# Kernel optimization log

Measured on AMD Instinct MI355X. Metric: run time of the kernel, lower is better.

The kernel has to match this reference:

```python
import jax, jax.numpy as jnp
import numpy as np

B, MAXN, D, H, S = 64, 512, 512, 8, 32
DH = D // H          # per-head dim = 64
N = B * MAXN         # 32768 total nodes
E = 524288           # ~avg degree 16
EPS = 1e-5


def setup_inputs() -> dict:
    key = jax.random.key(0)
    ks = jax.random.split(key, 18)
    s = 0.05
    x_dense = jax.random.normal(ks[0], (B, MAXN, D), jnp.float32)
    x = jax.random.normal(ks[1], (N, D), jnp.float32)
    src = jax.random.randint(ks[2], (E,), 0, N)
    # destinations kept within the same graph as the source
    dst = (src // MAXN) * MAXN + jax.random.randint(ks[3], (E,), 0, MAXN)
    edge_index = jnp.stack([src, dst]).astype(jnp.int32)
    batch = (jnp.arange(N) // MAXN).astype(jnp.int32)  # sorted, 512 nodes/graph
    seed = jax.random.normal(ks[4], (S, 1, D), jnp.float32) * s
    # per-head GCN conv weights concatenated along output dim: [D, H*DH] == [D, D]
    Wk = jax.random.normal(ks[5], (D, D), jnp.float32) * s
    bk = jnp.zeros((D,), jnp.float32)
    Wv = jax.random.normal(ks[6], (D, D), jnp.float32) * s
    bv = jnp.zeros((D,), jnp.float32)
    q_proj_weight = jax.random.normal(ks[7], (D, D), jnp.float32) * s
    Wo = jax.random.normal(ks[8], (D, D), jnp.float32) * s
    bo = jnp.zeros((D,), jnp.float32)
    Wff = jax.random.normal(ks[9], (D, D), jnp.float32) * s
    bff = jnp.zeros((D,), jnp.float32)
    gamma_h = jnp.ones((D,), jnp.float32)
    beta_h = jnp.zeros((D,), jnp.float32)
    gamma_z = jnp.ones((D,), jnp.float32)
    beta_z = jnp.zeros((D,), jnp.float32)
    return dict(x_dense=x_dense, x=x, edge_index=edge_index, batch=batch,
                seed=seed, Wk=Wk, bk=bk, Wv=Wv, bv=bv,
                q_proj_weight=q_proj_weight, Wo=Wo, bo=bo, Wff=Wff, bff=bff,
                gamma_h=gamma_h, beta_h=beta_h, gamma_z=gamma_z, beta_z=beta_z)


def _gcn(x, W, b, src, dst):
    # PyG GCNConv with self-loops + symmetric norm; all H heads fused via W [D, H*DH]
    xw = x @ W                                   # [N, D]
    idx = jnp.arange(N)
    src_f = jnp.concatenate([src, idx])
    dst_f = jnp.concatenate([dst, idx])
    deg = jax.ops.segment_sum(jnp.ones_like(dst_f, dtype=x.dtype), dst_f, num_segments=N)
    dinv = jax.lax.rsqrt(deg)                    # deg >= 1 (self-loops)
    norm = dinv[src_f] * dinv[dst_f]             # [E+N]
    out = jax.ops.segment_sum(xw[src_f] * norm[:, None], dst_f, num_segments=N)
    return out + b


def _to_dense(feat, batch):
    # to_dense_batch for sorted batch vector; padded slots are zeros
    counts = jax.ops.segment_sum(jnp.ones((N,), jnp.int32), batch, num_segments=B)
    start = jnp.cumsum(counts) - counts
    pos = jnp.arange(N) - start[batch]
    return jnp.zeros((B, MAXN, feat.shape[-1]), feat.dtype).at[batch, pos].set(feat)


def _layernorm(x, g, b):
    m = jnp.mean(x, -1, keepdims=True)
    v = jnp.mean(jnp.square(x - m), -1, keepdims=True)
    return (x - m) * jax.lax.rsqrt(v + EPS) * g + b


def reference(x_dense, x, edge_index, batch, seed, Wk, bk, Wv, bv,
              q_proj_weight, Wo, bo, Wff, bff, gamma_h, beta_h, gamma_z, beta_z):
    src, dst = edge_index[0], edge_index[1]
    k_nodes = _gcn(x, Wk, bk, src, dst)          # [N, D] (H heads concat)
    v_nodes = _gcn(x, Wv, bv, src, dst)
    k_dense = _to_dense(k_nodes, batch)          # [B, MAXN, D]
    v_dense = _to_dense(v_nodes, batch)

    # query: seed [S,1,D] repeated over batch -> [S,B,D]; q projection (F.linear)
    query = jnp.broadcast_to(seed, (S, B, D))
    q = jnp.einsum('sbd,ed->sbe', query, q_proj_weight)
    scale = 1.0 / jnp.sqrt(jnp.float32(DH))
    qh = (q * scale).reshape(S, B, H, DH).transpose(1, 2, 0, 3)     # [B,H,S,DH]
    kh = k_dense.reshape(B, MAXN, H, DH).transpose(0, 2, 1, 3)      # [B,H,N,DH]
    vh = v_dense.reshape(B, MAXN, H, DH).transpose(0, 2, 1, 3)
    scores = jnp.einsum('bhsd,bhnd->bhsn', qh, kh)                  # [B,H,S,MAXN]
    attn = jax.nn.softmax(scores, axis=-1)                          # no padding mask (faithful)
    ctx = jnp.einsum('bhsn,bhnd->bhsd', attn, vh)                   # [B,H,S,DH]
    ctx = ctx.transpose(0, 2, 1, 3).reshape(B, S, D)                # heads concat
    attn_out = ctx @ Wo.T + bo                                      # [B,S,D]

    query_bse = jnp.broadcast_to(seed.transpose(1, 0, 2), (B, S, D))
    embed = _layernorm(query_bse + attn_out, gamma_h, beta_h)
    embed = _layernorm(embed + embed @ Wff.T + bff, gamma_z, beta_z)
    return embed
```

## Files before the change

kernel.cpp:

```cpp
#include <hip/hip_runtime.h>
#include <hip/hip_bf16.h>

#define BN   64
#define MAXN 512
#define DIM  512
#define NH   8
#define NS   32
#define NN   32768
#define NE   524288
#define MP   (2048 * 512)

typedef __hip_bfloat16 bf16;
using bf16x8 = __attribute__((ext_vector_type(8))) short;
using f32x4  = __attribute__((ext_vector_type(4))) float;

__device__ int   g_cnt[NN];
__device__ int   g_cur[NN];
__device__ int   g_off[NN + 1];
__device__ int   g_csr[NE];
__device__ float g_dinv[NN];
__device__ bf16  g_xb[NN * DIM];
__device__ bf16  g_agg[NN * DIM];
__device__ bf16  g_aggT[NN * DIM];
__device__ bf16  g_qf[256 * DIM];
__device__ bf16  g_wob[DIM * DIM];
__device__ bf16  g_wvb[DIM * DIM];
__device__ bf16  g_wvo[DIM * 8 * DIM];
__device__ float g_bvo[DIM];
__device__ bf16  g_wffT[DIM * DIM];
__device__ float g_q[NS * DIM];
__device__ bf16  g_sc[BN * 256 * MAXN];
__device__ bf16  g_cp[BN * NS * 8 * DIM];
__device__ float g_part[8 * MP];
__device__ float g_h1[BN * NS * DIM];
__device__ bf16  g_h1b[BN * NS * DIM];

__device__ inline float bf2f(unsigned short u) {
    union { unsigned int i; float f; } x; x.i = ((unsigned int)u) << 16; return x.f;
}

__device__ inline void gll16(const bf16* g, bf16* l) {
    __builtin_amdgcn_global_load_lds(
        (const __attribute__((address_space(1))) void*)g,
        (__attribute__((address_space(3))) void*)l, 16, 0, 0);
}

__global__ void k_zero() {
    int i = blockIdx.x * 256 + threadIdx.x;
    if (i < NN) { g_cnt[i] = 0; g_cur[i] = 0; }
}

__global__ void k_count(const int* __restrict__ dst) {
    int e = blockIdx.x * 256 + threadIdx.x;
    if (e < NE) atomicAdd(&g_cnt[dst[e]], 1);
}

__global__ void k_scan() {
    __shared__ int part[1024];
    int t = threadIdx.x;
    int base = t * 32;
    int loc[32]; int s = 0;
#pragma unroll
    for (int i = 0; i < 32; i++) { loc[i] = g_cnt[base + i]; s += loc[i]; }
    part[t] = s; __syncthreads();
    for (int o = 1; o < 1024; o <<= 1) {
        int v = (t >= o) ? part[t - o] : 0;
        __syncthreads();
        part[t] += v;
        __syncthreads();
    }
    int ex = (t == 0) ? 0 : part[t - 1];
#pragma unroll
    for (int i = 0; i < 32; i++) {
        g_off[base + i] = ex; ex += loc[i];
        g_dinv[base + i] = rsqrtf(1.0f + (float)loc[i]);
    }
    if (t == 1023) g_off[NN] = ex;
}

__global__ void k_fill(const int* __restrict__ src, const int* __restrict__ dst) {
    int e = blockIdx.x * 256 + threadIdx.x;
    if (e < NE) {
        int d = dst[e];
        int p = atomicAdd(&g_cur[d], 1);
        g_csr[g_off[d] + p] = src[e];
    }
}

__global__ __launch_bounds__(256) void k_xb(const float* __restrict__ x) {
    long i = (long)(blockIdx.x * 256 + threadIdx.x) * 8;
    int node = (int)(i >> 9);
    float w = g_dinv[node];
    float4 a = *(const float4*)(x + i);
    float4 b = *(const float4*)(x + i + 4);
    float v[8] = {a.x, a.y, a.z, a.w, b.x, b.y, b.z, b.w};
    bf16x8 o;
#pragma unroll
    for (int j = 0; j < 8; j++) { bf16 t = __float2bfloat16(v[j] * w); o[j] = *(short*)&t; }
    *(bf16x8*)(g_xb + i) = o;
}

__global__ __launch_bounds__(256) void k_gather() {
    int bid = blockIdx.x;
    int lb = (bid & 7) * 1024 + (bid >> 3);
    int wave = threadIdx.x >> 6, lane = threadIdx.x & 63;
    int node = lb * 4 + wave;

    bf16x8 sv = ((const bf16x8*)(g_xb + (long)node * DIM))[lane];
    float acc[8];
#pragma unroll
    for (int j = 0; j < 8; j++) acc[j] = bf2f((unsigned short)sv[j]);

    int e = g_off[node], e1 = g_off[node + 1];
    for (; e + 4 <= e1; e += 4) {
        int s0 = g_csr[e], s1 = g_csr[e + 1], s2 = g_csr[e + 2], s3 = g_csr[e + 3];
        bf16x8 r0 = ((const bf16x8*)(g_xb + (long)s0 * DIM))[lane];
        bf16x8 r1 = ((const bf16x8*)(g_xb + (long)s1 * DIM))[lane];
        bf16x8 r2 = ((const bf16x8*)(g_xb + (long)s2 * DIM))[lane];
        bf16x8 r3 = ((const bf16x8*)(g_xb + (long)s3 * DIM))[lane];
#pragma unroll
        for (int j = 0; j < 8; j++)
            acc[j] += (bf2f((unsigned short)r0[j]) + bf2f((unsigned short)r1[j]))
                    + (bf2f((unsigned short)r2[j]) + bf2f((unsigned short)r3[j]));
    }
    for (; e < e1; e++) {
        int s0 = g_csr[e];
        bf16x8 r0 = ((const bf16x8*)(g_xb + (long)s0 * DIM))[lane];
#pragma unroll
        for (int j = 0; j < 8; j++) acc[j] += bf2f((unsigned short)r0[j]);
    }
    float dd = g_dinv[node];
    bf16x8 o;
#pragma unroll
    for (int j = 0; j < 8; j++) { bf16 t = __float2bfloat16(acc[j] * dd); o[j] = *(short*)&t; }
    ((bf16x8*)(g_agg + (long)node * DIM))[lane] = o;
}

__global__ __launch_bounds__(256) void k_aggT() {
    __shared__ unsigned short L[64][72];
    int id = blockIdx.x;
    int b = id >> 6, t = id & 63;
    int n0 = (t & 7) * 64, d0 = (t >> 3) * 64;
    int tid = threadIdx.x;
    const unsigned short* src = (const unsigned short*)g_agg + ((long)b * 512 + n0) * 512 + d0;
#pragma unroll
    for (int p = 0; p < 2; p++) {
        int r = (tid >> 3) + 32 * p, c = (tid & 7) * 8;
        *(int4*)&L[r][c] = *(const int4*)(src + (long)r * 512 + c);
    }
    __syncthreads();
    unsigned short* dst = (unsigned short*)g_aggT + ((long)b * 512 + d0) * 512 + n0;
#pragma unroll
    for (int p = 0; p < 2; p++) {
        int dr = (tid >> 3) + 32 * p, c0 = (tid & 7) * 8;
        unsigned short tmp[8];
#pragma unroll
        for (int j = 0; j < 8; j++) tmp[j] = L[c0 + j][dr];
        *(int4*)(dst + (long)dr * 512 + c0) = *(int4*)tmp;
    }
}

__global__ void k_qproj(const float* __restrict__ seed, const float* __restrict__ Wq) {
    int i = blockIdx.x * 256 + threadIdx.x;
    int s = i >> 9, e = i & 511;
    const float* sr = seed + s * DIM;
    const float* wr = Wq + e * DIM;
    float a0 = 0.f, a1 = 0.f;
    for (int d = 0; d < DIM; d += 8) {
        float4 a = *(const float4*)(sr + d);
        float4 b = *(const float4*)(wr + d);
        float4 c = *(const float4*)(sr + d + 4);
        float4 w = *(const float4*)(wr + d + 4);
        a0 += a.x * b.x + a.y * b.y + a.z * b.z + a.w * b.w;
        a1 += c.x * w.x + c.y * w.y + c.z * w.z + c.w * w.w;
    }
    g_q[i] = (a0 + a1) * 0.125f;
}

__global__ __launch_bounds__(256) void k_cvt(const float* __restrict__ Wo,
                                             const float* __restrict__ Wv,
                                             const float* __restrict__ Wff) {
    long t = blockIdx.x * 256 + threadIdx.x;
    const float* src; bf16* dst; long off;
    if (t < 32768)      { src = Wo;  dst = g_wob;  off = t; }
    else if (t < 65536) { src = Wv;  dst = g_wvb;  off = t - 32768; }
    else                { src = Wff; dst = g_wffT; off = t - 65536; }
    long i = off * 8;
    float4 a = *(const float4*)(src + i);
    float4 b = *(const float4*)(src + i + 4);
    float v[8] = {a.x, a.y, a.z, a.w, b.x, b.y, b.z, b.w};
    bf16x8 o;
#pragma unroll
    for (int j = 0; j < 8; j++) { bf16 q = __float2bfloat16(v[j]); o[j] = *(short*)&q; }
    *(bf16x8*)(dst + i) = o;
}

__global__ __launch_bounds__(256) void k_qf(const float* __restrict__ Wk) {
    int i = blockIdx.x * 256 + threadIdx.x;
    int hs = i >> 9, d = i & 511;
    int h = hs >> 5, s = hs & 31;
    const float* qr = g_q + s * DIM + h * 64;
    const float* wr = Wk + d * DIM + h * 64;
    float a0 = 0.f, a1 = 0.f;
    for (int t2 = 0; t2 < 64; t2 += 8) {
        float4 a = *(const float4*)(qr + t2);
        float4 w = *(const float4*)(wr + t2);
        float4 c = *(const float4*)(qr + t2 + 4);
        float4 u = *(const float4*)(wr + t2 + 4);
        a0 += a.x * w.x + a.y * w.y + a.z * w.z + a.w * w.w;
        a1 += c.x * u.x + c.y * u.y + c.z * u.z + c.w * u.w;
    }
    g_qf[i] = __float2bfloat16(a0 + a1);
}

__global__ __launch_bounds__(256) void k_bvo(const float* __restrict__ bo,
                                             const float* __restrict__ bv,
                                             const float* __restrict__ Wo) {
    int e = blockIdx.x * 256 + threadIdx.x;
    const float* orow = Wo + (long)e * DIM;
    float a0 = 0.f, a1 = 0.f;
    for (int c = 0; c < DIM; c += 8) {
        float4 a = *(const float4*)(bv + c);
        float4 w = *(const float4*)(orow + c);
        float4 x = *(const float4*)(bv + c + 4);
        float4 u = *(const float4*)(orow + c + 4);
        a0 += a.x * w.x + a.y * w.y + a.z * w.z + a.w * w.w;
        a1 += x.x * u.x + x.y * u.y + x.z * u.z + x.w * u.w;
    }
    g_bvo[e] = bo[e] + a0 + a1;
}

__device__ __forceinline__ void gemm128(const bf16* __restrict__ A, long lda,
                                        const bf16* __restrict__ Bt, long ldb,
                                        long row0, long col0, int kbeg, int kend,
                                        bf16 (*As)[128 * 32], bf16 (*Bs)[128 * 32],
                                        f32x4 acc[4][4]) {
    int tid = threadIdx.x;
    int lane = tid & 63, wave = tid >> 6;
    int wr = wave >> 1, wc = wave & 1;
    int fr = lane & 15, fq = lane >> 4;
    int rchunk = (fq ^ ((fr >> 1) & 3)) * 8;
    int u0 = wave * 128 + lane;
    int sr0 = u0 >> 2, sc0 = ((u0 & 3) ^ ((sr0 >> 1) & 3)) * 8;
    int u1 = u0 + 64;
    int sr1 = u1 >> 2, sc1 = ((u1 & 3) ^ ((sr1 >> 1) & 3)) * 8;

    auto stage = [&](int buf, int kt) {
        gll16(A + (row0 + sr0) * lda + kt + sc0, As[buf] + u0 * 8);
        gll16(A + (row0 + sr1) * lda + kt + sc1, As[buf] + u1 * 8);
        gll16(Bt + (col0 + sr0) * ldb + kt + sc0, Bs[buf] + u0 * 8);
        gll16(Bt + (col0 + sr1) * ldb + kt + sc1, Bs[buf] + u1 * 8);
    };

    stage(0, kbeg);
    __syncthreads();
    for (int kt = kbeg; kt < kend; kt += 32) {
        int buf = ((kt - kbeg) >> 5) & 1;
        if (kt + 32 < kend) stage(buf ^ 1, kt + 32);
        bf16x8 af[4], bfv[4];
#pragma unroll
        for (int mi = 0; mi < 4; mi++)
            af[mi] = *(const bf16x8*)(As[buf] + (wr * 64 + mi * 16 + fr) * 32 + rchunk);
#pragma unroll
        for (int ni = 0; ni < 4; ni++)
            bfv[ni] = *(const bf16x8*)(Bs[buf] + (wc * 64 + ni * 16 + fr) * 32 + rchunk);
#pragma unroll
        for (int mi = 0; mi < 4; mi++)
#pragma unroll
            for (int ni = 0; ni < 4; ni++)
                acc[mi][ni] = __builtin_amdgcn_mfma_f32_16x16x32_bf16(af[mi], bfv[ni], acc[mi][ni], 0, 0, 0);
        __syncthreads();
    }
}

#define GEMM_PROLOGUE                                        \
    __shared__ bf16 As[2][128 * 32];                         \
    __shared__ bf16 Bs[2][128 * 32];                         \
    f32x4 acc[4][4];                                         \
    _Pragma("unroll")                                        \
    for (int i = 0; i < 4; i++)                              \
        _Pragma("unroll")                                    \
        for (int j = 0; j < 4; j++) acc[i][j] = (f32x4){0.f, 0.f, 0.f, 0.f}; \
    int lane = threadIdx.x & 63, wave = threadIdx.x >> 6;    \
    int wr = wave >> 1, wc = wave & 1;                       \
    int fr = lane & 15, fq = lane >> 4;

__global__ __launch_bounds__(256) void k_wvo() {
    GEMM_PROLOGUE
    int h = blockIdx.z;
    long row0 = (long)blockIdx.x * 128, col0 = (long)blockIdx.y * 128;
    gemm128(g_wob, DIM, g_wvb, DIM, row0, col0, h * 64, h * 64 + 64, As, Bs, acc);
#pragma unroll
    for (int mi = 0; mi < 4; mi++)
#pragma unroll
        for (int ni = 0; ni < 4; ni++) {
            long col = col0 + wc * 64 + ni * 16 + fr;
#pragma unroll
            for (int r = 0; r < 4; r++) {
                long row = row0 + wr * 64 + mi * 16 + fq * 4 + r;
                g_wvo[row * 4096 + h * 512 + col] = __float2bfloat16(acc[mi][ni][r]);
            }
        }
}

__global__ __launch_bounds__(256) void k_scores() {
    GEMM_PROLOGUE
    int b = blockIdx.z;
    long row0 = (long)blockIdx.x * 128, col0 = (long)blockIdx.y * 128;
    gemm128(g_qf, DIM, g_agg + (long)b * (MAXN * DIM), DIM, row0, col0, 0, DIM, As, Bs, acc);
    bf16* out = g_sc + (long)b * (256 * MAXN);
#pragma unroll
    for (int mi = 0; mi < 4; mi++)
#pragma unroll
        for (int ni = 0; ni < 4; ni++) {
            long col = col0 + wc * 64 + ni * 16 + fr;
#pragma unroll
            for (int r = 0; r < 4; r++) {
                long row = row0 + wr * 64 + mi * 16 + fq * 4 + r;
                out[row * MAXN + col] = __float2bfloat16(acc[mi][ni][r]);
            }
        }
}

__global__ __launch_bounds__(256) void k_soft() {
    int w = threadIdx.x >> 6, lane = threadIdx.x & 63;
    unsigned short* base = (unsigned short*)g_sc + ((long)blockIdx.x * 16 + w * 4) * MAXN;
#pragma unroll
    for (int r = 0; r < 4; r++) {
        unsigned short* row = base + (long)r * MAXN;
        float v[8]; float m = -1e30f;
#pragma unroll
        for (int k = 0; k < 8; k++) { v[k] = bf2f(row[lane + 64 * k]); m = fmaxf(m, v[k]); }
#pragma unroll
        for (int o = 32; o > 0; o >>= 1) m = fmaxf(m, __shfl_xor(m, o));
        float sum = 0.f;
#pragma unroll
        for (int k = 0; k < 8; k++) { v[k] = __expf(v[k] - m); sum += v[k]; }
#pragma unroll
        for (int o = 32; o > 0; o >>= 1) sum += __shfl_xor(sum, o);
        float inv = 1.0f / sum;
#pragma unroll
        for (int k = 0; k < 8; k++) {
            bf16 t = __float2bfloat16(v[k] * inv);
            row[lane + 64 * k] = *(unsigned short*)&t;
        }
    }
}

__global__ __launch_bounds__(256) void k_pvg() {
    GEMM_PROLOGUE
    int z = blockIdx.z, b = z >> 1, dh = z & 1;
    long row0 = (long)blockIdx.x * 128, col0 = (long)blockIdx.y * 128;
    gemm128(g_sc + (long)b * (256 * MAXN), MAXN,
            g_aggT + (long)b * (DIM * MAXN) + (long)dh * (256 * MAXN), MAXN,
            row0, col0, 0, MAXN, As, Bs, acc);
#pragma unroll
    for (int mi = 0; mi < 4; mi++)
#pragma unroll
        for (int ni = 0; ni < 4; ni++) {
            long col = col0 + wc * 64 + ni * 16 + fr;
#pragma unroll
            for (int r = 0; r < 4; r++) {
                long row = row0 + wr * 64 + mi * 16 + fq * 4 + r;
                g_cp[((long)b * NS + (row & 31)) * 4096 + (row >> 5) * 512 + dh * 256 + col] =
                    __float2bfloat16(acc[mi][ni][r]);
            }
        }
}

__global__ __launch_bounds__(256) void k_vo() {
    GEMM_PROLOGUE
    int z = blockIdx.z;
    long row0 = (long)blockIdx.x * 128, col0 = (long)blockIdx.y * 128;
    gemm128(g_cp, 4096, g_wvo, 4096, row0, col0, z * 512, z * 512 + 512, As, Bs, acc);
    float* out = g_part + (long)z * MP;
#pragma unroll
    for (int mi = 0; mi < 4; mi++)
#pragma unroll
        for (int ni = 0; ni < 4; ni++) {
            long col = col0 + wc * 64 + ni * 16 + fr;
#pragma unroll
            for (int r = 0; r < 4; r++) {
                long row = row0 + wr * 64 + mi * 16 + fq * 4 + r;
                out[row * DIM + col] = acc[mi][ni][r];
            }
        }
}

__global__ __launch_bounds__(256) void k_ffn() {
    GEMM_PROLOGUE
    int z = blockIdx.z;
    long row0 = (long)blockIdx.x * 128, col0 = (long)blockIdx.y * 128;
    gemm128(g_h1b, DIM, g_wffT, DIM, row0, col0, z * 128, z * 128 + 128, As, Bs, acc);
    float* out = g_part + (long)z * MP;
#pragma unroll
    for (int mi = 0; mi < 4; mi++)
#pragma unroll
        for (int ni = 0; ni < 4; ni++) {
            long col = col0 + wc * 64 + ni * 16 + fr;
#pragma unroll
            for (int r = 0; r < 4; r++) {
                long row = row0 + wr * 64 + mi * 16 + fq * 4 + r;
                out[row * DIM + col] = acc[mi][ni][r];
            }
        }
}

__device__ inline float blockReduceSum(float v, float* red, int tid) {
#pragma unroll
    for (int o = 32; o > 0; o >>= 1) v += __shfl_xor(v, o);
    __syncthreads();
    if ((tid & 63) == 0) red[tid >> 6] = v;
    __syncthreads();
    return red[0] + red[1] + red[2] + red[3];
}

__global__ __launch_bounds__(256) void k_ln1(const float* __restrict__ seed,
                                             const float* __restrict__ gamma,
                                             const float* __restrict__ beta) {
    __shared__ float red[4];
    int r = blockIdx.x, t = threadIdx.x;
    int s = r & 31;
    long base = (long)r * DIM;
    float v0 = seed[s * DIM + t] + g_bvo[t];
    float v1 = seed[s * DIM + 256 + t] + g_bvo[256 + t];
#pragma unroll
    for (int z = 0; z < 8; z++) {
        v0 += g_part[(long)z * MP + base + t];
        v1 += g_part[(long)z * MP + base + 256 + t];
    }
    float mean = blockReduceSum(v0 + v1, red, t) * (1.0f / DIM);
    float d0 = v0 - mean, d1 = v1 - mean;
    float var = blockReduceSum(d0 * d0 + d1 * d1, red, t) * (1.0f / DIM);
    float ri = rsqrtf(var + 1e-5f);
    float o0 = d0 * ri * gamma[t] + beta[t];
    float o1 = d1 * ri * gamma[256 + t] + beta[256 + t];
    g_h1[base + t] = o0; g_h1[base + 256 + t] = o1;
    g_h1b[base + t] = __float2bfloat16(o0);
    g_h1b[base + 256 + t] = __float2bfloat16(o1);
}

__global__ __launch_bounds__(256) void k_ln2(const float* __restrict__ gamma,
                                             const float* __restrict__ beta,
                                             const float* __restrict__ bff,
                                             float* __restrict__ out) {
    __shared__ float red[4];
    int r = blockIdx.x, t = threadIdx.x;
    long base = (long)r * DIM;
    float v0 = g_h1[base + t] + bff[t];
    float v1 = g_h1[base + 256 + t] + bff[256 + t];
#pragma unroll
    for (int z = 0; z < 4; z++) {
        v0 += g_part[(long)z * MP + base + t];
        v1 += g_part[(long)z * MP + base + 256 + t];
    }
    float mean = blockReduceSum(v0 + v1, red, t) * (1.0f / DIM);
    float d0 = v0 - mean, d1 = v1 - mean;
    float var = blockReduceSum(d0 * d0 + d1 * d1, red, t) * (1.0f / DIM);
    float ri = rsqrtf(var + 1e-5f);
    out[base + t] = d0 * ri * gamma[t] + beta[t];
    out[base + 256 + t] = d1 * ri * gamma[256 + t] + beta[256 + t];
}

extern "C" void kernel_launch(void* const* d_in, const int* in_sizes, int n_in,
                              void* d_out, int out_size, void* d_ws, size_t ws_size,
                              hipStream_t stream) {
    (void)in_sizes; (void)n_in; (void)out_size; (void)d_ws; (void)ws_size;
    const float* x    = (const float*)d_in[1];
    const int*   ei   = (const int*)d_in[2];
    const int*   esrc = ei;
    const int*   edst = ei + NE;
    const float* seed = (const float*)d_in[4];
    const float* Wk   = (const float*)d_in[5];
    const float* Wv   = (const float*)d_in[7];
    const float* bv   = (const float*)d_in[8];
    const float* Wq   = (const float*)d_in[9];
    const float* Wo   = (const float*)d_in[10];
    const float* bo   = (const float*)d_in[11];
    const float* Wff  = (const float*)d_in[12];
    const float* bff  = (const float*)d_in[13];
    const float* gh   = (const float*)d_in[14];
    const float* bh   = (const float*)d_in[15];
    const float* gz   = (const float*)d_in[16];
    const float* bz   = (const float*)d_in[17];
    float* out = (float*)d_out;

    k_zero <<<NN / 256, 256, 0, stream>>>();
    k_count<<<NE / 256, 256, 0, stream>>>(edst);
    k_scan <<<1, 1024, 0, stream>>>();
    k_fill <<<NE / 256, 256, 0, stream>>>(esrc, edst);
    k_xb   <<<(NN * DIM) / (256 * 8), 256, 0, stream>>>(x);
    k_gather<<<NN / 4, 256, 0, stream>>>();
    k_aggT <<<BN * 64, 256, 0, stream>>>();
    k_qproj<<<(NS * DIM) / 256, 256, 0, stream>>>(seed, Wq);
    k_cvt  <<<384, 256, 0, stream>>>(Wo, Wv, Wff);
    k_qf   <<<512, 256, 0, stream>>>(Wk);
    k_wvo  <<<dim3(4, 4, 8), 256, 0, stream>>>();
    k_bvo  <<<2, 256, 0, stream>>>(bo, bv, Wo);

    k_scores<<<dim3(2, 4, BN), 256, 0, stream>>>();
    k_soft  <<<1024, 256, 0, stream>>>();
    k_pvg   <<<dim3(2, 2, BN * 2), 256, 0, stream>>>();

    k_vo <<<dim3(16, 4, 8), 256, 0, stream>>>();
    k_ln1<<<BN * NS, 256, 0, stream>>>(seed, gh, bh);
    k_ffn<<<dim3(16, 4, 4), 256, 0, stream>>>();
    k_ln2<<<BN * NS, 256, 0, stream>>>(gz, bz, bff, out);
}
```

Baseline: 270.5 us.

## Merge independent prep kernels into combined launches and halve split-K partials

Independent small kernels are merged into single launches that branch on block index: edge counting with q-projection, weight conversion and bias folding; CSR fill with x scaling, qf and the Wv·Wo GEMM; scores GEMM with the agg transpose. This cuts launch count and serialization gaps between tiny kernels. The k_vo split-K factor drops from 8 to 4, which halves partial-sum traffic in ln1 but lengthens each block's K loop. The gather loop is unrolled to 8 neighbours to raise memory-level parallelism.

```diff
diff --git a/kernel.cpp b/kernel.cpp
--- a/kernel.cpp
+++ b/kernel.cpp
@@ -31,7 +31,7 @@
 __device__ float g_q[NS * DIM];
 __device__ bf16  g_sc[BN * 256 * MAXN];
 __device__ bf16  g_cp[BN * NS * 8 * DIM];
-__device__ float g_part[8 * MP];
+__device__ float g_part[4 * MP];
 __device__ float g_h1[BN * NS * DIM];
 __device__ bf16  g_h1b[BN * NS * DIM];
 
@@ -50,9 +50,61 @@
     if (i < NN) { g_cnt[i] = 0; g_cur[i] = 0; }
 }
 
-__global__ void k_count(const int* __restrict__ dst) {
-    int e = blockIdx.x * 256 + threadIdx.x;
-    if (e < NE) atomicAdd(&g_cnt[dst[e]], 1);
+__global__ __launch_bounds__(256) void k_cntprep(const int* __restrict__ dst,
+                                                 const float* __restrict__ seed,
+                                                 const float* __restrict__ Wq,
+                                                 const float* __restrict__ Wo,
+                                                 const float* __restrict__ Wv,
+                                                 const float* __restrict__ Wff,
+                                                 const float* __restrict__ bo,
+                                                 const float* __restrict__ bv) {
+    int blk = blockIdx.x;
+    if (blk < 2048) {
+        int e = blk * 256 + threadIdx.x;
+        atomicAdd(&g_cnt[dst[e]], 1);
+    } else if (blk < 2112) {
+        int i = (blk - 2048) * 256 + threadIdx.x;
+        int s = i >> 9, e = i & 511;
+        const float* sr = seed + s * DIM;
+        const float* wr = Wq + e * DIM;
+        float a0 = 0.f, a1 = 0.f;
+        for (int d = 0; d < DIM; d += 8) {
+            float4 a = *(const float4*)(sr + d);
+            float4 b = *(const float4*)(wr + d);
+            float4 c = *(const float4*)(sr + d + 4);
+            float4 w = *(const float4*)(wr + d + 4);
+            a0 += a.x * b.x + a.y * b.y + a.z * b.z + a.w * b.w;
+            a1 += c.x * w.x + c.y * w.y + c.z * w.z + c.w * w.w;
+        }
+        g_q[i] = (a0 + a1) * 0.125f;
+    } else if (blk < 2496) {
+        long t = (long)(blk - 2112) * 256 + threadIdx.x;
+        const float* src; bf16* dstp; long off;
+        if (t < 32768)      { src = Wo;  dstp = g_wob;  off = t; }
+        else if (t < 65536) { src = Wv;  dstp = g_wvb;  off = t - 32768; }
+        else                { src = Wff; dstp = g_wffT; off = t - 65536; }
+        long i = off * 8;
+        float4 a = *(const float4*)(src + i);
+        float4 b = *(const float4*)(src + i + 4);
+        float v[8] = {a.x, a.y, a.z, a.w, b.x, b.y, b.z, b.w};
+        bf16x8 o;
+#pragma unroll
+        for (int j = 0; j < 8; j++) { bf16 q = __float2bfloat16(v[j]); o[j] = *(short*)&q; }
+        *(bf16x8*)(dstp + i) = o;
+    } else {
+        int e = (blk - 2496) * 256 + threadIdx.x;
+        const float* orow = Wo + (long)e * DIM;
+        float a0 = 0.f, a1 = 0.f;
+        for (int c = 0; c < DIM; c += 8) {
+            float4 a = *(const float4*)(bv + c);
+            float4 w = *(const float4*)(orow + c);
+            float4 xx = *(const float4*)(bv + c + 4);
+            float4 u = *(const float4*)(orow + c + 4);
+            a0 += a.x * w.x + a.y * w.y + a.z * w.z + a.w * w.w;
+            a1 += xx.x * u.x + xx.y * u.y + xx.z * u.z + xx.w * u.w;
+        }
+        g_bvo[e] = bo[e] + a0 + a1;
+    }
 }
 
 __global__ void k_scan() {
@@ -76,158 +128,6 @@
         g_dinv[base + i] = rsqrtf(1.0f + (float)loc[i]);
     }
     if (t == 1023) g_off[NN] = ex;
-}
-
-__global__ void k_fill(const int* __restrict__ src, const int* __restrict__ dst) {
-    int e = blockIdx.x * 256 + threadIdx.x;
-    if (e < NE) {
-        int d = dst[e];
-        int p = atomicAdd(&g_cur[d], 1);
-        g_csr[g_off[d] + p] = src[e];
-    }
-}
-
-__global__ __launch_bounds__(256) void k_xb(const float* __restrict__ x) {
-    long i = (long)(blockIdx.x * 256 + threadIdx.x) * 8;
-    int node = (int)(i >> 9);
-    float w = g_dinv[node];
-    float4 a = *(const float4*)(x + i);
-    float4 b = *(const float4*)(x + i + 4);
-    float v[8] = {a.x, a.y, a.z, a.w, b.x, b.y, b.z, b.w};
-    bf16x8 o;
-#pragma unroll
-    for (int j = 0; j < 8; j++) { bf16 t = __float2bfloat16(v[j] * w); o[j] = *(short*)&t; }
-    *(bf16x8*)(g_xb + i) = o;
-}
-
-__global__ __launch_bounds__(256) void k_gather() {
-    int bid = blockIdx.x;
-    int lb = (bid & 7) * 1024 + (bid >> 3);
-    int wave = threadIdx.x >> 6, lane = threadIdx.x & 63;
-    int node = lb * 4 + wave;
-
-    bf16x8 sv = ((const bf16x8*)(g_xb + (long)node * DIM))[lane];
-    float acc[8];
-#pragma unroll
-    for (int j = 0; j < 8; j++) acc[j] = bf2f((unsigned short)sv[j]);
-
-    int e = g_off[node], e1 = g_off[node + 1];
-    for (; e + 4 <= e1; e += 4) {
-        int s0 = g_csr[e], s1 = g_csr[e + 1], s2 = g_csr[e + 2], s3 = g_csr[e + 3];
-        bf16x8 r0 = ((const bf16x8*)(g_xb + (long)s0 * DIM))[lane];
-        bf16x8 r1 = ((const bf16x8*)(g_xb + (long)s1 * DIM))[lane];
-        bf16x8 r2 = ((const bf16x8*)(g_xb + (long)s2 * DIM))[lane];
-        bf16x8 r3 = ((const bf16x8*)(g_xb + (long)s3 * DIM))[lane];
-#pragma unroll
-        for (int j = 0; j < 8; j++)
-            acc[j] += (bf2f((unsigned short)r0[j]) + bf2f((unsigned short)r1[j]))
-                    + (bf2f((unsigned short)r2[j]) + bf2f((unsigned short)r3[j]));
-    }
-    for (; e < e1; e++) {
-        int s0 = g_csr[e];
-        bf16x8 r0 = ((const bf16x8*)(g_xb + (long)s0 * DIM))[lane];
-#pragma unroll
-        for (int j = 0; j < 8; j++) acc[j] += bf2f((unsigned short)r0[j]);
-    }
-    float dd = g_dinv[node];
-    bf16x8 o;
-#pragma unroll
-    for (int j = 0; j < 8; j++) { bf16 t = __float2bfloat16(acc[j] * dd); o[j] = *(short*)&t; }
-    ((bf16x8*)(g_agg + (long)node * DIM))[lane] = o;
-}
-
-__global__ __launch_bounds__(256) void k_aggT() {
-    __shared__ unsigned short L[64][72];
-    int id = blockIdx.x;
-    int b = id >> 6, t = id & 63;
-    int n0 = (t & 7) * 64, d0 = (t >> 3) * 64;
-    int tid = threadIdx.x;
-    const unsigned short* src = (const unsigned short*)g_agg + ((long)b * 512 + n0) * 512 + d0;
-#pragma unroll
-    for (int p = 0; p < 2; p++) {
-        int r = (tid >> 3) + 32 * p, c = (tid & 7) * 8;
-        *(int4*)&L[r][c] = *(const int4*)(src + (long)r * 512 + c);
-    }
-    __syncthreads();
-    unsigned short* dst = (unsigned short*)g_aggT + ((long)b * 512 + d0) * 512 + n0;
-#pragma unroll
-    for (int p = 0; p < 2; p++) {
-        int dr = (tid >> 3) + 32 * p, c0 = (tid & 7) * 8;
-        unsigned short tmp[8];
-#pragma unroll
-        for (int j = 0; j < 8; j++) tmp[j] = L[c0 + j][dr];
-        *(int4*)(dst + (long)dr * 512 + c0) = *(int4*)tmp;
-    }
-}
-
-__global__ void k_qproj(const float* __restrict__ seed, const float* __restrict__ Wq) {
-    int i = blockIdx.x * 256 + threadIdx.x;
-    int s = i >> 9, e = i & 511;
-    const float* sr = seed + s * DIM;
-    const float* wr = Wq + e * DIM;
-    float a0 = 0.f, a1 = 0.f;
-    for (int d = 0; d < DIM; d += 8) {
-        float4 a = *(const float4*)(sr + d);
-        float4 b = *(const float4*)(wr + d);
-        float4 c = *(const float4*)(sr + d + 4);
-        float4 w = *(const float4*)(wr + d + 4);
-        a0 += a.x * b.x + a.y * b.y + a.z * b.z + a.w * b.w;
-        a1 += c.x * w.x + c.y * w.y + c.z * w.z + c.w * w.w;
-    }
-    g_q[i] = (a0 + a1) * 0.125f;
-}
-
-__global__ __launch_bounds__(256) void k_cvt(const float* __restrict__ Wo,
-                                             const float* __restrict__ Wv,
-                                             const float* __restrict__ Wff) {
-    long t = blockIdx.x * 256 + threadIdx.x;
-    const float* src; bf16* dst; long off;
-    if (t < 32768)      { src = Wo;  dst = g_wob;  off = t; }
-    else if (t < 65536) { src = Wv;  dst = g_wvb;  off = t - 32768; }
-    else                { src = Wff; dst = g_wffT; off = t - 65536; }
-    long i = off * 8;
-    float4 a = *(const float4*)(src + i);
-    float4 b = *(const float4*)(src + i + 4);
-    float v[8] = {a.x, a.y, a.z, a.w, b.x, b.y, b.z, b.w};
-    bf16x8 o;
-#pragma unroll
-    for (int j = 0; j < 8; j++) { bf16 q = __float2bfloat16(v[j]); o[j] = *(short*)&q; }
-    *(bf16x8*)(dst + i) = o;
-}
-
-__global__ __launch_bounds__(256) void k_qf(const float* __restrict__ Wk) {
-    int i = blockIdx.x * 256 + threadIdx.x;
-    int hs = i >> 9, d = i & 511;
-    int h = hs >> 5, s = hs & 31;
-    const float* qr = g_q + s * DIM + h * 64;
-    const float* wr = Wk + d * DIM + h * 64;
-    float a0 = 0.f, a1 = 0.f;
-    for (int t2 = 0; t2 < 64; t2 += 8) {
-        float4 a = *(const float4*)(qr + t2);
-        float4 w = *(const float4*)(wr + t2);
-        float4 c = *(const float4*)(qr + t2 + 4);
-        float4 u = *(const float4*)(wr + t2 + 4);
-        a0 += a.x * w.x + a.y * w.y + a.z * w.z + a.w * w.w;
-        a1 += c.x * u.x + c.y * u.y + c.z * u.z + c.w * u.w;
-    }
-    g_qf[i] = __float2bfloat16(a0 + a1);
-}
-
-__global__ __launch_bounds__(256) void k_bvo(const float* __restrict__ bo,
-                                             const float* __restrict__ bv,
-                                             const float* __restrict__ Wo) {
-    int e = blockIdx.x * 256 + threadIdx.x;
-    const float* orow = Wo + (long)e * DIM;
-    float a0 = 0.f, a1 = 0.f;
-    for (int c = 0; c < DIM; c += 8) {
-        float4 a = *(const float4*)(bv + c);
-        float4 w = *(const float4*)(orow + c);
-        float4 x = *(const float4*)(bv + c + 4);
-        float4 u = *(const float4*)(orow + c + 4);
-        a0 += a.x * w.x + a.y * w.y + a.z * w.z + a.w * w.w;
-        a1 += x.x * u.x + x.y * u.y + x.z * u.z + x.w * u.w;
-    }
-    g_bvo[e] = bo[e] + a0 + a1;
 }
 
 __device__ __forceinline__ void gemm128(const bf16* __restrict__ A, long lda,
@@ -273,9 +173,7 @@
     }
 }
 
-#define GEMM_PROLOGUE                                        \
-    __shared__ bf16 As[2][128 * 32];                         \
-    __shared__ bf16 Bs[2][128 * 32];                         \
+#define ACC_INIT                                             \
     f32x4 acc[4][4];                                         \
     _Pragma("unroll")                                        \
     for (int i = 0; i < 4; i++)                              \
@@ -285,41 +183,148 @@
     int wr = wave >> 1, wc = wave & 1;                       \
     int fr = lane & 15, fq = lane >> 4;
 
-__global__ __launch_bounds__(256) void k_wvo() {
-    GEMM_PROLOGUE
-    int h = blockIdx.z;
-    long row0 = (long)blockIdx.x * 128, col0 = (long)blockIdx.y * 128;
-    gemm128(g_wob, DIM, g_wvb, DIM, row0, col0, h * 64, h * 64 + 64, As, Bs, acc);
-#pragma unroll
-    for (int mi = 0; mi < 4; mi++)
-#pragma unroll
-        for (int ni = 0; ni < 4; ni++) {
-            long col = col0 + wc * 64 + ni * 16 + fr;
-#pragma unroll
-            for (int r = 0; r < 4; r++) {
-                long row = row0 + wr * 64 + mi * 16 + fq * 4 + r;
-                g_wvo[row * 4096 + h * 512 + col] = __float2bfloat16(acc[mi][ni][r]);
+__global__ __launch_bounds__(256) void k_fillxb(const int* __restrict__ src,
+                                                const int* __restrict__ dst,
+                                                const float* __restrict__ x,
+                                                const float* __restrict__ Wk) {
+    __shared__ bf16 As[2][128 * 32];
+    __shared__ bf16 Bs[2][128 * 32];
+    int blk = blockIdx.x;
+    if (blk < 2048) {
+        int e = blk * 256 + threadIdx.x;
+        int d = dst[e];
+        int p = atomicAdd(&g_cur[d], 1);
+        g_csr[g_off[d] + p] = src[e];
+    } else if (blk < 10240) {
+        long i = (long)(blk - 2048) * (256 * 8) + (long)threadIdx.x * 8;
+        int node = (int)(i >> 9);
+        float w = g_dinv[node];
+        float4 a = *(const float4*)(x + i);
+        float4 b = *(const float4*)(x + i + 4);
+        float v[8] = {a.x, a.y, a.z, a.w, b.x, b.y, b.z, b.w};
+        bf16x8 o;
+#pragma unroll
+        for (int j = 0; j < 8; j++) { bf16 t = __float2bfloat16(v[j] * w); o[j] = *(short*)&t; }
+        *(bf16x8*)(g_xb + i) = o;
+    } else if (blk < 10752) {
+        int i = (blk - 10240) * 256 + threadIdx.x;
+        int hs = i >> 9, d = i & 511;
+        int h = hs >> 5, s = hs & 31;
+        const float* qr = g_q + s * DIM + h * 64;
+        const float* wr = Wk + d * DIM + h * 64;
+        float a0 = 0.f, a1 = 0.f;
+        for (int t2 = 0; t2 < 64; t2 += 8) {
+            float4 a = *(const float4*)(qr + t2);
+            float4 w = *(const float4*)(wr + t2);
+            float4 c = *(const float4*)(qr + t2 + 4);
+            float4 u = *(const float4*)(wr + t2 + 4);
+            a0 += a.x * w.x + a.y * w.y + a.z * w.z + a.w * w.w;
+            a1 += c.x * u.x + c.y * u.y + c.z * u.z + c.w * u.w;
+        }
+        g_qf[i] = __float2bfloat16(a0 + a1);
+    } else {
+        int wi = blk - 10752;
+        int bx = wi & 3, by = (wi >> 2) & 3, h = wi >> 4;
+        ACC_INIT
+        long row0 = (long)bx * 128, col0 = (long)by * 128;
+        gemm128(g_wob, DIM, g_wvb, DIM, row0, col0, h * 64, h * 64 + 64, As, Bs, acc);
+#pragma unroll
+        for (int mi = 0; mi < 4; mi++)
+#pragma unroll
+            for (int ni = 0; ni < 4; ni++) {
+                long col = col0 + wc * 64 + ni * 16 + fr;
+#pragma unroll
+                for (int r = 0; r < 4; r++) {
+                    long row = row0 + wr * 64 + mi * 16 + fq * 4 + r;
+                    g_wvo[row * 4096 + h * 512 + col] = __float2bfloat16(acc[mi][ni][r]);
+                }
             }
-        }
-}
-
-__global__ __launch_bounds__(256) void k_scores() {
-    GEMM_PROLOGUE
-    int b = blockIdx.z;
-    long row0 = (long)blockIdx.x * 128, col0 = (long)blockIdx.y * 128;
-    gemm128(g_qf, DIM, g_agg + (long)b * (MAXN * DIM), DIM, row0, col0, 0, DIM, As, Bs, acc);
-    bf16* out = g_sc + (long)b * (256 * MAXN);
-#pragma unroll
-    for (int mi = 0; mi < 4; mi++)
-#pragma unroll
-        for (int ni = 0; ni < 4; ni++) {
-            long col = col0 + wc * 64 + ni * 16 + fr;
-#pragma unroll
-            for (int r = 0; r < 4; r++) {
-                long row = row0 + wr * 64 + mi * 16 + fq * 4 + r;
-                out[row * MAXN + col] = __float2bfloat16(acc[mi][ni][r]);
+    }
+}
+
+__global__ __launch_bounds__(256) void k_gather() {
+    int bid = blockIdx.x;
+    int lb = (bid & 7) * 1024 + (bid >> 3);
+    int wave = threadIdx.x >> 6, lane = threadIdx.x & 63;
+    int node = lb * 4 + wave;
+
+    bf16x8 sv = ((const bf16x8*)(g_xb + (long)node * DIM))[lane];
+    float acc[8];
+#pragma unroll
+    for (int j = 0; j < 8; j++) acc[j] = bf2f((unsigned short)sv[j]);
+
+    int e = g_off[node], e1 = g_off[node + 1];
+    for (; e + 8 <= e1; e += 8) {
+        bf16x8 r[8];
+#pragma unroll
+        for (int q = 0; q < 8; q++)
+            r[q] = ((const bf16x8*)(g_xb + (long)g_csr[e + q] * DIM))[lane];
+#pragma unroll
+        for (int j = 0; j < 8; j++) {
+            float s01 = bf2f((unsigned short)r[0][j]) + bf2f((unsigned short)r[1][j]);
+            float s23 = bf2f((unsigned short)r[2][j]) + bf2f((unsigned short)r[3][j]);
+            float s45 = bf2f((unsigned short)r[4][j]) + bf2f((unsigned short)r[5][j]);
+            float s67 = bf2f((unsigned short)r[6][j]) + bf2f((unsigned short)r[7][j]);
+            acc[j] += (s01 + s23) + (s45 + s67);
+        }
+    }
+    for (; e < e1; e++) {
+        bf16x8 r0 = ((const bf16x8*)(g_xb + (long)g_csr[e] * DIM))[lane];
+#pragma unroll
+        for (int j = 0; j < 8; j++) acc[j] += bf2f((unsigned short)r0[j]);
+    }
+    float dd = g_dinv[node];
+    bf16x8 o;
+#pragma unroll
+    for (int j = 0; j < 8; j++) { bf16 t = __float2bfloat16(acc[j] * dd); o[j] = *(short*)&t; }
+    ((bf16x8*)(g_agg + (long)node * DIM))[lane] = o;
+}
+
+__global__ __launch_bounds__(256) void k_aggsc() {
+    __shared__ __align__(16) char smem[32768];
+    int blk = blockIdx.x;
+    if (blk < 512) {
+        bf16 (*As)[128 * 32] = (bf16(*)[128 * 32])smem;
+        bf16 (*Bs)[128 * 32] = (bf16(*)[128 * 32])(smem + 16384);
+        int b = blk & 63, bx = (blk >> 6) & 1, by = blk >> 7;
+        ACC_INIT
+        long row0 = (long)bx * 128, col0 = (long)by * 128;
+        gemm128(g_qf, DIM, g_agg + (long)b * (MAXN * DIM), DIM, row0, col0, 0, DIM, As, Bs, acc);
+        bf16* out = g_sc + (long)b * (256 * MAXN);
+#pragma unroll
+        for (int mi = 0; mi < 4; mi++)
+#pragma unroll
+            for (int ni = 0; ni < 4; ni++) {
+                long col = col0 + wc * 64 + ni * 16 + fr;
+#pragma unroll
+                for (int r = 0; r < 4; r++) {
+                    long row = row0 + wr * 64 + mi * 16 + fq * 4 + r;
+                    out[row * MAXN + col] = __float2bfloat16(acc[mi][ni][r]);
+                }
             }
-        }
+    } else {
+        unsigned short (*L)[72] = (unsigned short(*)[72])smem;
+        int id = blk - 512;
+        int b = id >> 6, t = id & 63;
+        int n0 = (t & 7) * 64, d0 = (t >> 3) * 64;
+        int tid = threadIdx.x;
+        const unsigned short* src = (const unsigned short*)g_agg + ((long)b * 512 + n0) * 512 + d0;
+#pragma unroll
+        for (int p = 0; p < 2; p++) {
+            int r = (tid >> 3) + 32 * p, c = (tid & 7) * 8;
+            *(int4*)&L[r][c] = *(const int4*)(src + (long)r * 512 + c);
+        }
+        __syncthreads();
+        unsigned short* dst = (unsigned short*)g_aggT + ((long)b * 512 + d0) * 512 + n0;
+#pragma unroll
+        for (int p = 0; p < 2; p++) {
+            int dr = (tid >> 3) + 32 * p, c0 = (tid & 7) * 8;
+            unsigned short tmp[8];
+#pragma unroll
+            for (int j = 0; j < 8; j++) tmp[j] = L[c0 + j][dr];
+            *(int4*)(dst + (long)dr * 512 + c0) = *(int4*)tmp;
+        }
+    }
 }
 
 __global__ __launch_bounds__(256) void k_soft() {
@@ -348,9 +353,12 @@
 }
 
 __global__ __launch_bounds__(256) void k_pvg() {
-    GEMM_PROLOGUE
-    int z = blockIdx.z, b = z >> 1, dh = z & 1;
-    long row0 = (long)blockIdx.x * 128, col0 = (long)blockIdx.y * 128;
+    __shared__ bf16 As[2][128 * 32];
+    __shared__ bf16 Bs[2][128 * 32];
+    int blk = blockIdx.x;
+    int b = blk & 63, bx = (blk >> 6) & 1, by = (blk >> 7) & 1, dh = blk >> 8;
+    ACC_INIT
+    long row0 = (long)bx * 128, col0 = (long)by * 128;
     gemm128(g_sc + (long)b * (256 * MAXN), MAXN,
             g_aggT + (long)b * (DIM * MAXN) + (long)dh * (256 * MAXN), MAXN,
             row0, col0, 0, MAXN, As, Bs, acc);
@@ -369,10 +377,12 @@
 }
 
 __global__ __launch_bounds__(256) void k_vo() {
-    GEMM_PROLOGUE
+    __shared__ bf16 As[2][128 * 32];
+    __shared__ bf16 Bs[2][128 * 32];
+    ACC_INIT
     int z = blockIdx.z;
     long row0 = (long)blockIdx.x * 128, col0 = (long)blockIdx.y * 128;
-    gemm128(g_cp, 4096, g_wvo, 4096, row0, col0, z * 512, z * 512 + 512, As, Bs, acc);
+    gemm128(g_cp, 4096, g_wvo, 4096, row0, col0, z * 1024, z * 1024 + 1024, As, Bs, acc);
     float* out = g_part + (long)z * MP;
 #pragma unroll
     for (int mi = 0; mi < 4; mi++)
@@ -388,7 +398,9 @@
 }
 
 __global__ __launch_bounds__(256) void k_ffn() {
-    GEMM_PROLOGUE
+    __shared__ bf16 As[2][128 * 32];
+    __shared__ bf16 Bs[2][128 * 32];
+    ACC_INIT
     int z = blockIdx.z;
     long row0 = (long)blockIdx.x * 128, col0 = (long)blockIdx.y * 128;
     gemm128(g_h1b, DIM, g_wffT, DIM, row0, col0, z * 128, z * 128 + 128, As, Bs, acc);
@@ -425,7 +437,7 @@
     float v0 = seed[s * DIM + t] + g_bvo[t];
     float v1 = seed[s * DIM + 256 + t] + g_bvo[256 + t];
 #pragma unroll
-    for (int z = 0; z < 8; z++) {
+    for (int z = 0; z < 4; z++) {
         v0 += g_part[(long)z * MP + base + t];
         v1 += g_part[(long)z * MP + base + 256 + t];
     }
@@ -485,25 +497,16 @@
     const float* bz   = (const float*)d_in[17];
     float* out = (float*)d_out;
 
-    k_zero <<<NN / 256, 256, 0, stream>>>();
-    k_count<<<NE / 256, 256, 0, stream>>>(edst);
-    k_scan <<<1, 1024, 0, stream>>>();
-    k_fill <<<NE / 256, 256, 0, stream>>>(esrc, edst);
-    k_xb   <<<(NN * DIM) / (256 * 8), 256, 0, stream>>>(x);
-    k_gather<<<NN / 4, 256, 0, stream>>>();
-    k_aggT <<<BN * 64, 256, 0, stream>>>();
-    k_qproj<<<(NS * DIM) / 256, 256, 0, stream>>>(seed, Wq);
-    k_cvt  <<<384, 256, 0, stream>>>(Wo, Wv, Wff);
-    k_qf   <<<512, 256, 0, stream>>>(Wk);
-    k_wvo  <<<dim3(4, 4, 8), 256, 0, stream>>>();
-    k_bvo  <<<2, 256, 0, stream>>>(bo, bv, Wo);
-
-    k_scores<<<dim3(2, 4, BN), 256, 0, stream>>>();
-    k_soft  <<<1024, 256, 0, stream>>>();
-    k_pvg   <<<dim3(2, 2, BN * 2), 256, 0, stream>>>();
-
-    k_vo <<<dim3(16, 4, 8), 256, 0, stream>>>();
-    k_ln1<<<BN * NS, 256, 0, stream>>>(seed, gh, bh);
-    k_ffn<<<dim3(16, 4, 4), 256, 0, stream>>>();
-    k_ln2<<<BN * NS, 256, 0, stream>>>(gz, bz, bff, out);
-}
+    k_zero   <<<NN / 256, 256, 0, stream>>>();
+    k_cntprep<<<2498, 256, 0, stream>>>(edst, seed, Wq, Wo, Wv, Wff, bo, bv);
+    k_scan   <<<1, 1024, 0, stream>>>();
+    k_fillxb <<<10880, 256, 0, stream>>>(esrc, edst, x, Wk);
+    k_gather <<<NN / 4, 256, 0, stream>>>();
+    k_aggsc  <<<512 + BN * 64, 256, 0, stream>>>();
+    k_soft   <<<1024, 256, 0, stream>>>();
+    k_pvg    <<<512, 256, 0, stream>>>();
+    k_vo     <<<dim3(16, 4, 4), 256, 0, stream>>>();
+    k_ln1    <<<BN * NS, 256, 0, stream>>>(seed, gh, bh);
+    k_ffn    <<<dim3(16, 4, 4), 256, 0, stream>>>();
+    k_ln2    <<<BN * NS, 256, 0, stream>>>(gz, bz, bff, out);
+}
```

New measurement: 253.6 us. 6.3% less time.
